# Performance work log

Measured on AMD Instinct MI355X. Metric: run time of the kernel, lower is better.

## Reference

```python
import jax, jax.numpy as jnp
import numpy as np

N_RAYS = 8192
N_SAMPLES = 64   # timesteps per ray
HID = 128
BOOSTER = 1.0
FAR = 10.0


def rsh_cart_3(d):
    # real spherical harmonics, cartesian, degree 3 -> 16 coefficients
    x, y, z = d[..., 0], d[..., 1], d[..., 2]
    x2, y2, z2 = x * x, y * y, z * z
    return jnp.stack([
        jnp.full_like(x, 0.282094791773878),
        -0.488602511902920 * y,
        0.488602511902920 * z,
        -0.488602511902920 * x,
        1.092548430592079 * x * y,
        -1.092548430592079 * y * z,
        0.315391565252520 * (3.0 * z2 - 1.0),
        -1.092548430592079 * x * z,
        0.546274215296040 * (x2 - y2),
        -0.590043589926644 * y * (3.0 * x2 - y2),
        2.890611442640554 * x * y * z,
        -0.457045799464466 * y * (5.0 * z2 - 1.0),
        0.373176332590115 * z * (5.0 * z2 - 3.0),
        -0.457045799464466 * x * (5.0 * z2 - 1.0),
        1.445305721320277 * z * (x2 - y2),
        -0.590043589926644 * x * (x2 - 3.0 * y2),
    ], axis=-1)


def setup_inputs() -> dict:
    key = jax.random.key(0)
    ks = jax.random.split(key, 10)
    N, H = N_RAYS, HID

    def w(k, shape, fan_in):
        return (jax.random.normal(k, shape, jnp.float32) / np.float32(np.sqrt(fan_in)))

    return dict(
        rays_o=jax.random.normal(ks[0], (N, 3), jnp.float32) * 0.3,
        rays_d=jax.random.normal(ks[1], (N, 3), jnp.float32),
        aabb=jnp.array([[-1.0, -1.0, -1.0], [1.0, 1.0, 1.0]], jnp.float32),
        W1=w(ks[2], (3, H), 3), b1=jnp.zeros((H,), jnp.float32),
        W2=w(ks[3], (H, H), H), b2=jnp.zeros((H,), jnp.float32),
        Wd=w(ks[4], (H, 1), H), bd=jnp.zeros((1,), jnp.float32),
        Wf=w(ks[5], (H, 16), H), bf=jnp.zeros((16,), jnp.float32),
        Wc1=w(ks[6], (32, H), 32), bc1=jnp.zeros((H,), jnp.float32),
        Wc2=w(ks[7], (H, 3), H), bc2=jnp.zeros((3,), jnp.float32),
    )


def reference(rays_o, rays_d, aabb, W1, b1, W2, b2, Wd, bd, Wf, bf, Wc1, bc1, Wc2, bc2):
    # --- ray / AABB intersection (slab test), as in RayBundle.intersect_aabb ---
    inv_d = 1.0 / rays_d
    t1 = (aabb[0] - rays_o) * inv_d
    t2 = (aabb[1] - rays_o) * inv_d
    tnear = jnp.maximum(jnp.max(jnp.minimum(t1, t2), -1), 0.0)      # (N,)
    tfar = jnp.minimum(jnp.min(jnp.maximum(t1, t2), -1), FAR)       # (N,)
    active = tnear < tfar                                           # active_mask()
    tnear = jnp.where(active, tnear, 0.0)
    tfar = jnp.where(active, tfar, 1.0)

    # --- timestep sampler: midpoint stratification between tnear/tfar ---
    T = N_SAMPLES
    frac = (jnp.arange(T, dtype=rays_o.dtype) + 0.5) / T
    ts = tnear[:, None] + frac[None, :] * (tfar - tnear)[:, None]    # (N,T)
    xyz = rays_o[:, None, :] + rays_d[:, None, :] * ts[..., None]    # (N,T,3)

    # --- convert_world_to_box_normalized + BoundsFilter.test ---
    xyz_ndc = (xyz - aabb[0]) / (aabb[1] - aabb[0]) * 2.0 - 1.0
    inside = jnp.all((xyz_ndc >= -1.0) & (xyz_ndc <= 1.0), -1)       # (N,T)

    # --- direction harmonics (rsh_cart_3 of normalized direction) ---
    dnorm = jnp.linalg.norm(rays_d, axis=-1, keepdims=True)          # (N,1)
    ynm = rsh_cart_3(rays_d / dnorm)                                 # (N,16)

    # --- radiance field MLP (query-everywhere; masked points contribute 0) ---
    h = jax.nn.relu(xyz_ndc @ W1 + b1)
    h = jax.nn.relu(h @ W2 + b2)
    sigma = jnp.exp(h @ Wd + bd)[..., 0]                             # (N,T) density
    feat = h @ Wf + bf                                               # (N,T,16)
    cond = jnp.broadcast_to(ynm[:, None, :], feat.shape)
    hc = jax.nn.relu(jnp.concatenate([feat, cond], -1) @ Wc1 + bc1)
    color = jax.nn.sigmoid(hc @ Wc2 + bc2)                           # (N,T,3)
    m = inside.astype(sigma.dtype)
    sigma = sigma * m                                                # scatter-zeros equiv
    color = color * m[..., None]

    # --- integrate_timesteps: transmittance * alpha weights ---
    tfinal = tfar + BOOSTER
    deltas = jnp.concatenate([ts[:, 1:] - ts[:, :-1], tfinal[:, None] - ts[:, -1:]], -1)
    tau = sigma * deltas * dnorm                                     # (N,T)
    excl = jnp.concatenate([jnp.zeros_like(tau[:, :1]), jnp.cumsum(tau[:, :-1], -1)], -1)
    weights = jnp.exp(-excl) * (1.0 - jnp.exp(-tau))                 # (N,T)

    # --- color_map / alpha_map / depth_map ---
    cmap = jnp.einsum('nt,ntc->nc', weights, color)                  # (N,3)
    amap = jnp.sum(weights, -1, keepdims=True)                       # (N,1)
    dmap = jnp.sum(weights * ts, -1, keepdims=True)                  # (N,1)
    am = active[:, None].astype(cmap.dtype)
    return jnp.concatenate([cmap * am, amap * am, dmap * am], -1)    # (N,5)
```

## Files before the change

### kernel.cpp

```cpp
#include <hip/hip_runtime.h>
#include <math.h>

#define THREADS 256
#define GRID 512
#define NRAYS 8192
#define FAR_T 10.0f
#define CSTR 24

typedef __attribute__((ext_vector_type(8))) short short8;
typedef __attribute__((ext_vector_type(4))) float f32x4;

static __device__ __forceinline__ unsigned f2bfu(float f) {
    unsigned u = __builtin_bit_cast(unsigned, f);
    return (u + 0x7fffu + ((u >> 16) & 1u)) >> 16;
}
static __device__ __forceinline__ unsigned pk2(float a, float b) {
    unsigned ra = __builtin_bit_cast(unsigned, a) + 0x8000u;
    unsigned rb = __builtin_bit_cast(unsigned, b) + 0x8000u;
    return __builtin_amdgcn_perm(rb, ra, 0x07060302u);
}
static __device__ __forceinline__ int sw128(int r, int k) { return (r << 7) + (k ^ ((r & 7) << 3)); }
static __device__ __forceinline__ int sw32(int r, int k)  { return (r << 5) + (k ^ ((r & 3) << 3)); }
static __device__ __forceinline__ f32x4 MFMA16(short8 a, short8 b, f32x4 c) {
    return __builtin_amdgcn_mfma_f32_16x16x32_bf16(a, b, c, 0, 0, 0);
}

struct RayP { float ox,oy,oz,dx,dy,dz,tn,tf,tstep,dnorm; bool act; };

static __device__ __forceinline__ RayP raySetup(const float* __restrict__ ro, const float* __restrict__ rd,
        int r, float a0x,float a0y,float a0z,float a1x,float a1y,float a1z) {
    RayP R;
    R.ox=ro[3*r+0]; R.oy=ro[3*r+1]; R.oz=ro[3*r+2];
    R.dx=rd[3*r+0]; R.dy=rd[3*r+1]; R.dz=rd[3*r+2];
    float ivx=1.f/R.dx, ivy=1.f/R.dy, ivz=1.f/R.dz;
    float t1x=(a0x-R.ox)*ivx, t2x=(a1x-R.ox)*ivx;
    float t1y=(a0y-R.oy)*ivy, t2y=(a1y-R.oy)*ivy;
    float t1z=(a0z-R.oz)*ivz, t2z=(a1z-R.oz)*ivz;
    float tn = fmaxf(fmaxf(fminf(t1x,t2x),fminf(t1y,t2y)),fminf(t1z,t2z));
    tn = fmaxf(tn, 0.f);
    float tf = fminf(fminf(fmaxf(t1x,t2x),fmaxf(t1y,t2y)),fmaxf(t1z,t2z));
    tf = fminf(tf, FAR_T);
    R.act = tn < tf;
    R.tn = R.act ? tn : 0.f;
    R.tf = R.act ? tf : 1.f;
    R.tstep = (R.tf - R.tn) * (1.f/64.f);
    R.dnorm = sqrtf(R.dx*R.dx + R.dy*R.dy + R.dz*R.dz);
    return R;
}

__global__ __launch_bounds__(THREADS)
__attribute__((amdgpu_waves_per_eu(2, 2), amdgpu_num_vgpr(256)))
void RadianceRenderer_kernel(const float* __restrict__ rays_o, const float* __restrict__ rays_d,
                             const float* __restrict__ aabb,
                             const float* __restrict__ W1, const float* __restrict__ b1,
                             const float* __restrict__ W2, const float* __restrict__ b2,
                             const float* __restrict__ Wd, const float* __restrict__ bd,
                             const float* __restrict__ Wf, const float* __restrict__ bf,
                             const float* __restrict__ Wc1, const float* __restrict__ bc1,
                             const float* __restrict__ Wc2, const float* __restrict__ bc2,
                             float* __restrict__ out)
{
    __shared__ __align__(16) short W1T[128*8];
    __shared__ __align__(16) short Wfd17[17*128];
    __shared__ __align__(16) short Wc2T3[3*128];
    __shared__ __align__(16) union {
        struct { short W2T[128*128]; short Wc1T[128*32]; } w;
        struct { short H1[128*128]; short H2[128*128]; short CC[128*CSTR];
                 short YNM[2*16]; float SIG[128]; float COL[128*4]; } a;
    } sm;

    const int tid  = threadIdx.x;
    const int lane = tid & 63;
    const int wv   = tid >> 6;
    const int l15  = lane & 15;
    const int l4   = lane >> 4;
    const short8 z8 = {0,0,0,0,0,0,0,0};

    for (int i = tid; i < 128*128; i += THREADS) {
        int k = i >> 7, n = i & 127;
        sm.w.W2T[sw128(n, k)] = (short)f2bfu(W2[i]);
    }
    for (int i = tid; i < 128*32; i += THREADS) {
        int n = i >> 5, k = i & 31;
        sm.w.Wc1T[sw32(n, k)] = (short)f2bfu(Wc1[k*128 + n]);
    }
    for (int i = tid; i < 17*128; i += THREADS) {
        int n = i >> 7, k = i & 127;
        float v = (n < 16) ? Wf[k*16 + n] : Wd[k];
        Wfd17[sw128(n, k)] = (short)f2bfu(v);
    }
    for (int i = tid; i < 3*128; i += THREADS) {
        int c = i >> 7, k = i & 127;
        Wc2T3[i] = (short)f2bfu(Wc2[k*3 + c]);
    }
    for (int i = tid; i < 128*8; i += THREADS) {
        int ch = i >> 3, k = i & 7;
        float f = (k < 3) ? W1[k*128 + ch] : ((k == 3) ? b1[ch] : 0.f);
        W1T[i] = (short)f2bfu(f);
    }
    __syncthreads();

    const int chB = (wv >> 1) * 64;
    const int smB = (wv & 1) * 64;
    const int sB3 = wv * 32;

    short8 w2f[4][4], wc1f[4];
    #pragma unroll
    for (int jn = 0; jn < 4; ++jn)
        #pragma unroll
        for (int kk = 0; kk < 4; ++kk)
            w2f[jn][kk] = *(const short8*)&sm.w.W2T[sw128(chB + 16*jn + l15, kk*32 + 8*l4)];
    #pragma unroll
    for (int cg = 0; cg < 4; ++cg)
        wc1f[cg] = *(const short8*)&sm.w.Wc1T[sw32(chB + 16*cg + l15, 8*l4)];

    float b2r[4][4], bc1r[4][4];
    #pragma unroll
    for (int jn = 0; jn < 4; ++jn)
        #pragma unroll
        for (int vv = 0; vv < 4; ++vv) {
            b2r[jn][vv]  = b2[chB + 16*jn + 4*l4 + vv];
            bc1r[jn][vv] = bc1[chB + 16*jn + 4*l4 + vv];
        }
    f32x4 bfv;
    #pragma unroll
    for (int vv = 0; vv < 4; ++vv) bfv[vv] = bf[4*l4 + vv];
    float bc2r[3] = { bc2[0], bc2[1], bc2[2] };
    const float bdr = bd[0];

    const float a0x=aabb[0],a0y=aabb[1],a0z=aabb[2],a1x=aabb[3],a1y=aabb[4],a1z=aabb[5];
    const float scx=2.f/(a1x-a0x), scy=2.f/(a1y-a0y), scz=2.f/(a1z-a0z);

    __syncthreads();

    for (int i = tid; i < 128*CSTR/2; i += THREADS) ((unsigned*)sm.a.CC)[i] = 0u;
    __syncthreads();

    int gp = -1;
    RayP Rp;

    for (int g = blockIdx.x; g < NRAYS/2; g += gridDim.x) {
        if (wv >= 2) {
            const int m   = tid - 128;
            const int ray = 2*g + (m >> 6);
            RayP R = raySetup(rays_o, rays_d, ray, a0x,a0y,a0z,a1x,a1y,a1z);
            const int s = m & 63;
            float t  = R.tn + ((float)s + 0.5f) * R.tstep;
            float px = fmaf(R.dx, t, R.ox);
            float py = fmaf(R.dy, t, R.oy);
            float pz = fmaf(R.dz, t, R.oz);
            float nx = fmaf(px - a0x, scx, -1.f);
            float ny = fmaf(py - a0y, scy, -1.f);
            float nz = fmaf(pz - a0z, scz, -1.f);
            *(uint2*)&sm.a.CC[m*CSTR] = make_uint2(pk2(nx, ny), pk2(nz, 1.0f));
            if (s == 0) {
                float inorm = 1.f / R.dnorm;
                float x = R.dx*inorm, y = R.dy*inorm, z = R.dz*inorm;
                float x2 = x*x, y2 = y*y, z2 = z*z;
                unsigned q0 = pk2(0.282094791773878f,              -0.488602511902920f*y);
                unsigned q1 = pk2(0.488602511902920f*z,            -0.488602511902920f*x);
                unsigned q2 = pk2(1.092548430592079f*x*y,          -1.092548430592079f*y*z);
                unsigned q3 = pk2(0.315391565252520f*(3.f*z2-1.f), -1.092548430592079f*x*z);
                unsigned q4 = pk2(0.546274215296040f*(x2-y2),      -0.590043589926644f*y*(3.f*x2-y2));
                unsigned q5 = pk2(2.890611442640554f*x*y*z,        -0.457045799464466f*y*(5.f*z2-1.f));
                unsigned q6 = pk2(0.373176332590115f*z*(5.f*z2-3.f), -0.457045799464466f*x*(5.f*z2-1.f));
                unsigned q7 = pk2(1.445305721320277f*z*(x2-y2),    -0.590043589926644f*x*(x2-3.f*y2));
                *(uint4*)&sm.a.YNM[(m >> 6)*16    ] = make_uint4(q0,q1,q2,q3);
                *(uint4*)&sm.a.YNM[(m >> 6)*16 + 8] = make_uint4(q4,q5,q6,q7);
            }
        } else if (gp >= 0) {
            const RayP R = Rp;
            const int m = wv*64 + lane;
            const int mx = (m >> 2) & 3;
            float t  = R.tn + ((float)lane + 0.5f) * R.tstep;
            float px = fmaf(R.dx, t, R.ox);
            float py = fmaf(R.dy, t, R.oy);
            float pz = fmaf(R.dz, t, R.oz);
            float nx = fmaf(px - a0x, scx, -1.f);
            float ny = fmaf(py - a0y, scy, -1.f);
            float nz = fmaf(pz - a0z, scz, -1.f);
            bool ins = (nx >= -1.f) & (nx <= 1.f) & (ny >= -1.f) & (ny <= 1.f)
                     & (nz >= -1.f) & (nz <= 1.f);
            float sig = ins ? __expf(sm.a.SIG[m] + bdr) : 0.f;
            float delta = (lane == 63) ? (R.tf + 1.0f - t) : R.tstep;
            float tau = sig * delta * R.dnorm;
            float cum = tau;
            #pragma unroll
            for (int off = 1; off < 64; off <<= 1) {
                float tmp = __shfl_up(cum, off);
                if (lane >= off) cum += tmp;
            }
            float excl = cum - tau;
            float wgt = __expf(-excl) * (1.f - __expf(-tau));
            float c0 = wgt * sm.a.COL[m*4 + (0 ^ mx)];
            float c1 = wgt * sm.a.COL[m*4 + (1 ^ mx)];
            float c2 = wgt * sm.a.COL[m*4 + (2 ^ mx)];
            float amv = wgt;
            float dmv = wgt * t;
            #pragma unroll
            for (int off = 32; off; off >>= 1) {
                c0  += __shfl_xor(c0,  off);
                c1  += __shfl_xor(c1,  off);
                c2  += __shfl_xor(c2,  off);
                amv += __shfl_xor(amv, off);
                dmv += __shfl_xor(dmv, off);
            }
            if (lane == 0) {
                float msk = R.act ? 1.f : 0.f;
                int ray = 2*gp + wv;
                out[ray*5+0] = c0*msk;
                out[ray*5+1] = c1*msk;
                out[ray*5+2] = c2*msk;
                out[ray*5+3] = amv*msk;
                out[ray*5+4] = dmv*msk;
            }
        }
        __syncthreads();

        {
            short8 bx[4];
            #pragma unroll
            for (int im = 0; im < 4; ++im) {
                short8 v = z8;
                if (l4 == 0) v = *(const short8*)&sm.a.CC[(smB + 16*im + l15)*CSTR];
                bx[im] = v;
            }
            #pragma unroll
            for (int jn = 0; jn < 4; ++jn) {
                short8 w1fr = z8;
                if (l4 == 0) w1fr = *(const short8*)&W1T[(chB + 16*jn + l15)*8];
                #pragma unroll
                for (int im = 0; im < 4; ++im) {
                    f32x4 v = MFMA16(w1fr, bx[im], (f32x4){0.f,0.f,0.f,0.f});
                    int m  = smB + 16*im + l15;
                    int n0 = chB + 16*jn + 4*l4;
                    float r0 = fmaxf(v[0], 0.f), r1 = fmaxf(v[1], 0.f);
                    float r2 = fmaxf(v[2], 0.f), r3 = fmaxf(v[3], 0.f);
                    *(uint2*)&sm.a.H1[sw128(m, n0)] = make_uint2(pk2(r0,r1), pk2(r2,r3));
                }
            }
        }
        __syncthreads();

        {
            f32x4 acc[4][4];
            #pragma unroll
            for (int jn = 0; jn < 4; ++jn)
                #pragma unroll
                for (int im = 0; im < 4; ++im)
                    acc[jn][im] = (f32x4){b2r[jn][0], b2r[jn][1], b2r[jn][2], b2r[jn][3]};
            #pragma unroll
            for (int kk = 0; kk < 4; ++kk) {
                short8 bfr[4];
                #pragma unroll
                for (int im = 0; im < 4; ++im)
                    bfr[im] = *(const short8*)&sm.a.H1[sw128(smB + 16*im + l15, kk*32 + 8*l4)];
                #pragma unroll
                for (int jn = 0; jn < 4; ++jn)
                    #pragma unroll
                    for (int im = 0; im < 4; ++im)
                        acc[jn][im] = MFMA16(w2f[jn][kk], bfr[im], acc[jn][im]);
            }
            #pragma unroll
            for (int jn = 0; jn < 4; ++jn)
                #pragma unroll
                for (int im = 0; im < 4; ++im) {
                    int m  = smB + 16*im + l15;
                    int n0 = chB + 16*jn + 4*l4;
                    f32x4 v = acc[jn][im];
                    float r0 = fmaxf(v[0], 0.f), r1 = fmaxf(v[1], 0.f);
                    float r2 = fmaxf(v[2], 0.f), r3 = fmaxf(v[3], 0.f);
                    *(uint2*)&sm.a.H2[sw128(m, n0)] = make_uint2(pk2(r0,r1), pk2(r2,r3));
                }
        }
        __syncthreads();

        {
            f32x4 f30[2] = { bfv, bfv };
            f32x4 f31[2] = { (f32x4){0,0,0,0}, (f32x4){0,0,0,0} };
            #pragma unroll
            for (int kk = 0; kk < 4; ++kk) {
                short8 bA = *(const short8*)&sm.a.H2[sw128(sB3 +      l15, kk*32 + 8*l4)];
                short8 bB = *(const short8*)&sm.a.H2[sw128(sB3 + 16 + l15, kk*32 + 8*l4)];
                short8 wfd0 = *(const short8*)&Wfd17[sw128(l15, kk*32 + 8*l4)];
                short8 wfd1 = z8;
                if (l15 == 0) wfd1 = *(const short8*)&Wfd17[sw128(16, kk*32 + 8*l4)];
                f30[0] = MFMA16(wfd0, bA, f30[0]);
                f30[1] = MFMA16(wfd0, bB, f30[1]);
                f31[0] = MFMA16(wfd1, bA, f31[0]);
                f31[1] = MFMA16(wfd1, bB, f31[1]);
            }
            #pragma unroll
            for (int sg = 0; sg < 2; ++sg) {
                int m = sB3 + 16*sg + l15;
                f32x4 v = f30[sg];
                *(uint2*)&sm.a.CC[m*CSTR + 4*l4] = make_uint2(pk2(v[0],v[1]), pk2(v[2],v[3]));
                if (l4 == 0) sm.a.SIG[m] = f31[sg][0];
            }
        }
        __syncthreads();

        {
            short8 bcc[4];
            #pragma unroll
            for (int sg = 0; sg < 4; ++sg) {
                int m = smB + 16*sg + l15;
                if (l4 < 2) bcc[sg] = *(const short8*)&sm.a.CC[m*CSTR + 8*l4];
                else        bcc[sg] = *(const short8*)&sm.a.YNM[(m >> 6)*16 + 8*(l4 - 2)];
            }
            #pragma unroll
            for (int cg = 0; cg < 4; ++cg)
                #pragma unroll
                for (int sg = 0; sg < 4; ++sg) {
                    f32x4 v = MFMA16(wc1f[cg], bcc[sg],
                                     (f32x4){bc1r[cg][0], bc1r[cg][1], bc1r[cg][2], bc1r[cg][3]});
                    int m  = smB + 16*sg + l15;
                    int n0 = chB + 16*cg + 4*l4;
                    float r0 = fmaxf(v[0], 0.f), r1 = fmaxf(v[1], 0.f);
                    float r2 = fmaxf(v[2], 0.f), r3 = fmaxf(v[3], 0.f);
                    *(uint2*)&sm.a.H1[sw128(m, n0)] = make_uint2(pk2(r0,r1), pk2(r2,r3));
                }
        }
        __syncthreads();

        {
            f32x4 c5[2] = { (f32x4){0,0,0,0}, (f32x4){0,0,0,0} };
            #pragma unroll
            for (int kk = 0; kk < 4; ++kk) {
                short8 wc2fr = z8;
                if (l15 < 3) wc2fr = *(const short8*)&Wc2T3[l15*128 + kk*32 + 8*l4];
                #pragma unroll
                for (int sg = 0; sg < 2; ++sg) {
                    short8 b = *(const short8*)&sm.a.H1[sw128(sB3 + 16*sg + l15, kk*32 + 8*l4)];
                    c5[sg] = MFMA16(wc2fr, b, c5[sg]);
                }
            }
            if (l4 == 0) {
                #pragma unroll
                for (int sg = 0; sg < 2; ++sg) {
                    int m = sB3 + 16*sg + l15;
                    int mx = (m >> 2) & 3;
                    #pragma unroll
                    for (int vv = 0; vv < 3; ++vv)
                        sm.a.COL[m*4 + (vv ^ mx)] = 1.f / (1.f + __expf(-(c5[sg][vv] + bc2r[vv])));
                }
            }
        }
        __syncthreads();

        if (wv < 2) Rp = raySetup(rays_o, rays_d, 2*g + wv, a0x,a0y,a0z,a1x,a1y,a1z);
        gp = g;
    }

    if (gp >= 0 && wv < 2) {
        const RayP R = Rp;
        const int m = wv*64 + lane;
        const int mx = (m >> 2) & 3;
        float t  = R.tn + ((float)lane + 0.5f) * R.tstep;
        float px = fmaf(R.dx, t, R.ox);
        float py = fmaf(R.dy, t, R.oy);
        float pz = fmaf(R.dz, t, R.oz);
        float nx = fmaf(px - a0x, scx, -1.f);
        float ny = fmaf(py - a0y, scy, -1.f);
        float nz = fmaf(pz - a0z, scz, -1.f);
        bool ins = (nx >= -1.f) & (nx <= 1.f) & (ny >= -1.f) & (ny <= 1.f)
                 & (nz >= -1.f) & (nz <= 1.f);
        float sig = ins ? __expf(sm.a.SIG[m] + bdr) : 0.f;
        float delta = (lane == 63) ? (R.tf + 1.0f - t) : R.tstep;
        float tau = sig * delta * R.dnorm;
        float cum = tau;
        #pragma unroll
        for (int off = 1; off < 64; off <<= 1) {
            float tmp = __shfl_up(cum, off);
            if (lane >= off) cum += tmp;
        }
        float excl = cum - tau;
        float wgt = __expf(-excl) * (1.f - __expf(-tau));
        float c0 = wgt * sm.a.COL[m*4 + (0 ^ mx)];
        float c1 = wgt * sm.a.COL[m*4 + (1 ^ mx)];
        float c2 = wgt * sm.a.COL[m*4 + (2 ^ mx)];
        float amv = wgt;
        float dmv = wgt * t;
        #pragma unroll
        for (int off = 32; off; off >>= 1) {
            c0  += __shfl_xor(c0,  off);
            c1  += __shfl_xor(c1,  off);
            c2  += __shfl_xor(c2,  off);
            amv += __shfl_xor(amv, off);
            dmv += __shfl_xor(dmv, off);
        }
        if (lane == 0) {
            float msk = R.act ? 1.f : 0.f;
            int ray = 2*gp + wv;
            out[ray*5+0] = c0*msk;
            out[ray*5+1] = c1*msk;
            out[ray*5+2] = c2*msk;
            out[ray*5+3] = amv*msk;
            out[ray*5+4] = dmv*msk;
        }
    }
}

extern "C" void kernel_launch(void* const* d_in, const int* in_sizes, int n_in,
                              void* d_out, int out_size, void* d_ws, size_t ws_size,
                              hipStream_t stream) {
    (void)in_sizes; (void)n_in; (void)d_ws; (void)ws_size; (void)out_size;
    const float* rays_o = (const float*)d_in[0];
    const float* rays_d = (const float*)d_in[1];
    const float* aabb   = (const float*)d_in[2];
    const float* W1  = (const float*)d_in[3];
    const float* b1  = (const float*)d_in[4];
    const float* W2  = (const float*)d_in[5];
    const float* b2  = (const float*)d_in[6];
    const float* Wd  = (const float*)d_in[7];
    const float* bd  = (const float*)d_in[8];
    const float* Wf  = (const float*)d_in[9];
    const float* bf  = (const float*)d_in[10];
    const float* Wc1 = (const float*)d_in[11];
    const float* bc1 = (const float*)d_in[12];
    const float* Wc2 = (const float*)d_in[13];
    const float* bc2 = (const float*)d_in[14];
    float* out = (float*)d_out;

    hipLaunchKernelGGL(RadianceRenderer_kernel, dim3(GRID), dim3(THREADS), 0, stream,
                       rays_o, rays_d, aabb, W1, b1, W2, b2, Wd, bd,
                       Wf, bf, Wc1, bc1, Wc2, bc2, out);
}
```

Before: 164.9 us.

## Double block to 512 threads, halve per-wave MFMA tiles, move biases to LDS

Raises the block from 4 to 8 waves and splits each GEMM's output channels across twice as many waves, so each wave holds half as many W2/Wc1 fragments and accumulators. Bias vectors now live in shared memory instead of registers. Color and sigma are stored in a planar CS array, and the SH coefficients are folded into unused CC padding. The ray setup is recomputed instead of carried across iterations. The goal is lower register pressure and more waves to hide latency, at the cost of more LDS traffic and idle waves in the per-ray stages.

```diff
diff --git a/kernel.cpp b/kernel.cpp
--- a/kernel.cpp
+++ b/kernel.cpp
@@ -1,7 +1,7 @@
 #include <hip/hip_runtime.h>
 #include <math.h>
 
-#define THREADS 256
+#define THREADS 512
 #define GRID 512
 #define NRAYS 8192
 #define FAR_T 10.0f
@@ -48,8 +48,7 @@
     return R;
 }
 
-__global__ __launch_bounds__(THREADS)
-__attribute__((amdgpu_waves_per_eu(2, 2), amdgpu_num_vgpr(256)))
+__global__ __launch_bounds__(THREADS, 4)
 void RadianceRenderer_kernel(const float* __restrict__ rays_o, const float* __restrict__ rays_d,
                              const float* __restrict__ aabb,
                              const float* __restrict__ W1, const float* __restrict__ b1,
@@ -63,10 +62,13 @@
     __shared__ __align__(16) short W1T[128*8];
     __shared__ __align__(16) short Wfd17[17*128];
     __shared__ __align__(16) short Wc2T3[3*128];
+    __shared__ __align__(16) float B2F[128];
+    __shared__ __align__(16) float BC1F[128];
     __shared__ __align__(16) union {
         struct { short W2T[128*128]; short Wc1T[128*32]; } w;
-        struct { short H1[128*128]; short H2[128*128]; short CC[128*CSTR];
-                 short YNM[2*16]; float SIG[128]; float COL[128*4]; } a;
+        struct { short H1[128*128]; short H2[128*128];
+                 short CC[128*CSTR];
+                 float CS[4*128]; } a;
     } sm;
 
     const int tid  = threadIdx.x;
@@ -98,30 +100,23 @@
         float f = (k < 3) ? W1[k*128 + ch] : ((k == 3) ? b1[ch] : 0.f);
         W1T[i] = (short)f2bfu(f);
     }
+    for (int i = tid; i < 128; i += THREADS) { B2F[i] = b2[i]; BC1F[i] = bc1[i]; }
     __syncthreads();
 
-    const int chB = (wv >> 1) * 64;
+    const int chB = (wv >> 1) * 32;
     const int smB = (wv & 1) * 64;
-    const int sB3 = wv * 32;
-
-    short8 w2f[4][4], wc1f[4];
+    const int sB3 = wv * 16;
+
+    short8 w2f[2][4], wc1f[2];
     #pragma unroll
-    for (int jn = 0; jn < 4; ++jn)
+    for (int jn = 0; jn < 2; ++jn)
         #pragma unroll
         for (int kk = 0; kk < 4; ++kk)
             w2f[jn][kk] = *(const short8*)&sm.w.W2T[sw128(chB + 16*jn + l15, kk*32 + 8*l4)];
     #pragma unroll
-    for (int cg = 0; cg < 4; ++cg)
+    for (int cg = 0; cg < 2; ++cg)
         wc1f[cg] = *(const short8*)&sm.w.Wc1T[sw32(chB + 16*cg + l15, 8*l4)];
 
-    float b2r[4][4], bc1r[4][4];
-    #pragma unroll
-    for (int jn = 0; jn < 4; ++jn)
-        #pragma unroll
-        for (int vv = 0; vv < 4; ++vv) {
-            b2r[jn][vv]  = b2[chB + 16*jn + 4*l4 + vv];
-            bc1r[jn][vv] = bc1[chB + 16*jn + 4*l4 + vv];
-        }
     f32x4 bfv;
     #pragma unroll
     for (int vv = 0; vv < 4; ++vv) bfv[vv] = bf[4*l4 + vv];
@@ -137,11 +132,10 @@
     __syncthreads();
 
     int gp = -1;
-    RayP Rp;
 
     for (int g = blockIdx.x; g < NRAYS/2; g += gridDim.x) {
-        if (wv >= 2) {
-            const int m   = tid - 128;
+        if (wv == 4 || wv == 5) {
+            const int m   = tid - 256;
             const int ray = 2*g + (m >> 6);
             RayP R = raySetup(rays_o, rays_d, ray, a0x,a0y,a0z,a1x,a1y,a1z);
             const int s = m & 63;
@@ -165,13 +159,12 @@
                 unsigned q5 = pk2(2.890611442640554f*x*y*z,        -0.457045799464466f*y*(5.f*z2-1.f));
                 unsigned q6 = pk2(0.373176332590115f*z*(5.f*z2-3.f), -0.457045799464466f*x*(5.f*z2-1.f));
                 unsigned q7 = pk2(1.445305721320277f*z*(x2-y2),    -0.590043589926644f*x*(x2-3.f*y2));
-                *(uint4*)&sm.a.YNM[(m >> 6)*16    ] = make_uint4(q0,q1,q2,q3);
-                *(uint4*)&sm.a.YNM[(m >> 6)*16 + 8] = make_uint4(q4,q5,q6,q7);
-            }
-        } else if (gp >= 0) {
-            const RayP R = Rp;
+                *(uint4*)&sm.a.CC[m*CSTR + 16]        = make_uint4(q0,q1,q2,q3);
+                *(uint4*)&sm.a.CC[(m+1)*CSTR + 16]    = make_uint4(q4,q5,q6,q7);
+            }
+        } else if (wv < 2 && gp >= 0) {
+            RayP R = raySetup(rays_o, rays_d, 2*gp + wv, a0x,a0y,a0z,a1x,a1y,a1z);
             const int m = wv*64 + lane;
-            const int mx = (m >> 2) & 3;
             float t  = R.tn + ((float)lane + 0.5f) * R.tstep;
             float px = fmaf(R.dx, t, R.ox);
             float py = fmaf(R.dy, t, R.oy);
@@ -181,7 +174,7 @@
             float nz = fmaf(pz - a0z, scz, -1.f);
             bool ins = (nx >= -1.f) & (nx <= 1.f) & (ny >= -1.f) & (ny <= 1.f)
                      & (nz >= -1.f) & (nz <= 1.f);
-            float sig = ins ? __expf(sm.a.SIG[m] + bdr) : 0.f;
+            float sig = ins ? __expf(sm.a.CS[3*128 + m] + bdr) : 0.f;
             float delta = (lane == 63) ? (R.tf + 1.0f - t) : R.tstep;
             float tau = sig * delta * R.dnorm;
             float cum = tau;
@@ -192,9 +185,9 @@
             }
             float excl = cum - tau;
             float wgt = __expf(-excl) * (1.f - __expf(-tau));
-            float c0 = wgt * sm.a.COL[m*4 + (0 ^ mx)];
-            float c1 = wgt * sm.a.COL[m*4 + (1 ^ mx)];
-            float c2 = wgt * sm.a.COL[m*4 + (2 ^ mx)];
+            float c0 = wgt * sm.a.CS[0*128 + m];
+            float c1 = wgt * sm.a.CS[1*128 + m];
+            float c2 = wgt * sm.a.CS[2*128 + m];
             float amv = wgt;
             float dmv = wgt * t;
             #pragma unroll
@@ -226,7 +219,7 @@
                 bx[im] = v;
             }
             #pragma unroll
-            for (int jn = 0; jn < 4; ++jn) {
+            for (int jn = 0; jn < 2; ++jn) {
                 short8 w1fr = z8;
                 if (l4 == 0) w1fr = *(const short8*)&W1T[(chB + 16*jn + l15)*8];
                 #pragma unroll
@@ -243,26 +236,23 @@
         __syncthreads();
 
         {
-            f32x4 acc[4][4];
-            #pragma unroll
-            for (int jn = 0; jn < 4; ++jn)
-                #pragma unroll
-                for (int im = 0; im < 4; ++im)
-                    acc[jn][im] = (f32x4){b2r[jn][0], b2r[jn][1], b2r[jn][2], b2r[jn][3]};
-            #pragma unroll
-            for (int kk = 0; kk < 4; ++kk) {
-                short8 bfr[4];
-                #pragma unroll
-                for (int im = 0; im < 4; ++im)
-                    bfr[im] = *(const short8*)&sm.a.H1[sw128(smB + 16*im + l15, kk*32 + 8*l4)];
-                #pragma unroll
-                for (int jn = 0; jn < 4; ++jn)
-                    #pragma unroll
-                    for (int im = 0; im < 4; ++im)
-                        acc[jn][im] = MFMA16(w2f[jn][kk], bfr[im], acc[jn][im]);
-            }
-            #pragma unroll
-            for (int jn = 0; jn < 4; ++jn)
+            f32x4 acc[2][4];
+            #pragma unroll
+            for (int jn = 0; jn < 2; ++jn) {
+                f32x4 bias = *(const f32x4*)&B2F[chB + 16*jn + 4*l4];
+                #pragma unroll
+                for (int im = 0; im < 4; ++im) acc[jn][im] = bias;
+            }
+            #pragma unroll
+            for (int kk = 0; kk < 4; ++kk)
+                #pragma unroll
+                for (int im = 0; im < 4; ++im) {
+                    short8 bfr = *(const short8*)&sm.a.H1[sw128(smB + 16*im + l15, kk*32 + 8*l4)];
+                    acc[0][im] = MFMA16(w2f[0][kk], bfr, acc[0][im]);
+                    acc[1][im] = MFMA16(w2f[1][kk], bfr, acc[1][im]);
+                }
+            #pragma unroll
+            for (int jn = 0; jn < 2; ++jn)
                 #pragma unroll
                 for (int im = 0; im < 4; ++im) {
                     int m  = smB + 16*im + l15;
@@ -276,27 +266,20 @@
         __syncthreads();
 
         {
-            f32x4 f30[2] = { bfv, bfv };
-            f32x4 f31[2] = { (f32x4){0,0,0,0}, (f32x4){0,0,0,0} };
+            f32x4 f30 = bfv;
+            f32x4 f31 = (f32x4){0.f,0.f,0.f,0.f};
+            const int m = sB3 + l15;
             #pragma unroll
             for (int kk = 0; kk < 4; ++kk) {
-                short8 bA = *(const short8*)&sm.a.H2[sw128(sB3 +      l15, kk*32 + 8*l4)];
-                short8 bB = *(const short8*)&sm.a.H2[sw128(sB3 + 16 + l15, kk*32 + 8*l4)];
+                short8 bA = *(const short8*)&sm.a.H2[sw128(m, kk*32 + 8*l4)];
                 short8 wfd0 = *(const short8*)&Wfd17[sw128(l15, kk*32 + 8*l4)];
                 short8 wfd1 = z8;
                 if (l15 == 0) wfd1 = *(const short8*)&Wfd17[sw128(16, kk*32 + 8*l4)];
-                f30[0] = MFMA16(wfd0, bA, f30[0]);
-                f30[1] = MFMA16(wfd0, bB, f30[1]);
-                f31[0] = MFMA16(wfd1, bA, f31[0]);
-                f31[1] = MFMA16(wfd1, bB, f31[1]);
-            }
-            #pragma unroll
-            for (int sg = 0; sg < 2; ++sg) {
-                int m = sB3 + 16*sg + l15;
-                f32x4 v = f30[sg];
-                *(uint2*)&sm.a.CC[m*CSTR + 4*l4] = make_uint2(pk2(v[0],v[1]), pk2(v[2],v[3]));
-                if (l4 == 0) sm.a.SIG[m] = f31[sg][0];
-            }
+                f30 = MFMA16(wfd0, bA, f30);
+                f31 = MFMA16(wfd1, bA, f31);
+            }
+            *(uint2*)&sm.a.CC[m*CSTR + 4*l4] = make_uint2(pk2(f30[0],f30[1]), pk2(f30[2],f30[3]));
+            if (l4 == 0) sm.a.CS[3*128 + m] = f31[0];
         }
         __syncthreads();
 
@@ -306,56 +289,48 @@
             for (int sg = 0; sg < 4; ++sg) {
                 int m = smB + 16*sg + l15;
                 if (l4 < 2) bcc[sg] = *(const short8*)&sm.a.CC[m*CSTR + 8*l4];
-                else        bcc[sg] = *(const short8*)&sm.a.YNM[(m >> 6)*16 + 8*(l4 - 2)];
-            }
-            #pragma unroll
-            for (int cg = 0; cg < 4; ++cg)
+                else        bcc[sg] = *(const short8*)&sm.a.CC[((m >> 6)*64 + (l4 - 2))*CSTR + 16];
+            }
+            #pragma unroll
+            for (int cg = 0; cg < 2; ++cg) {
+                f32x4 bias = *(const f32x4*)&BC1F[chB + 16*cg + 4*l4];
                 #pragma unroll
                 for (int sg = 0; sg < 4; ++sg) {
-                    f32x4 v = MFMA16(wc1f[cg], bcc[sg],
-                                     (f32x4){bc1r[cg][0], bc1r[cg][1], bc1r[cg][2], bc1r[cg][3]});
+                    f32x4 v = MFMA16(wc1f[cg], bcc[sg], bias);
                     int m  = smB + 16*sg + l15;
                     int n0 = chB + 16*cg + 4*l4;
                     float r0 = fmaxf(v[0], 0.f), r1 = fmaxf(v[1], 0.f);
                     float r2 = fmaxf(v[2], 0.f), r3 = fmaxf(v[3], 0.f);
                     *(uint2*)&sm.a.H1[sw128(m, n0)] = make_uint2(pk2(r0,r1), pk2(r2,r3));
                 }
+            }
         }
         __syncthreads();
 
         {
-            f32x4 c5[2] = { (f32x4){0,0,0,0}, (f32x4){0,0,0,0} };
+            f32x4 c5 = (f32x4){0.f,0.f,0.f,0.f};
+            const int m = sB3 + l15;
             #pragma unroll
             for (int kk = 0; kk < 4; ++kk) {
                 short8 wc2fr = z8;
                 if (l15 < 3) wc2fr = *(const short8*)&Wc2T3[l15*128 + kk*32 + 8*l4];
-                #pragma unroll
-                for (int sg = 0; sg < 2; ++sg) {
-                    short8 b = *(const short8*)&sm.a.H1[sw128(sB3 + 16*sg + l15, kk*32 + 8*l4)];
-                    c5[sg] = MFMA16(wc2fr, b, c5[sg]);
-                }
+                short8 b = *(const short8*)&sm.a.H1[sw128(m, kk*32 + 8*l4)];
+                c5 = MFMA16(wc2fr, b, c5);
             }
             if (l4 == 0) {
                 #pragma unroll
-                for (int sg = 0; sg < 2; ++sg) {
-                    int m = sB3 + 16*sg + l15;
-                    int mx = (m >> 2) & 3;
-                    #pragma unroll
-                    for (int vv = 0; vv < 3; ++vv)
-                        sm.a.COL[m*4 + (vv ^ mx)] = 1.f / (1.f + __expf(-(c5[sg][vv] + bc2r[vv])));
-                }
-            }
-        }
-        __syncthreads();
-
-        if (wv < 2) Rp = raySetup(rays_o, rays_d, 2*g + wv, a0x,a0y,a0z,a1x,a1y,a1z);
+                for (int vv = 0; vv < 3; ++vv)
+                    sm.a.CS[vv*128 + m] = 1.f / (1.f + __expf(-(c5[vv] + bc2r[vv])));
+            }
+        }
+        __syncthreads();
+
         gp = g;
     }
 
     if (gp >= 0 && wv < 2) {
-        const RayP R = Rp;
+        RayP R = raySetup(rays_o, rays_d, 2*gp + wv, a0x,a0y,a0z,a1x,a1y,a1z);
         const int m = wv*64 + lane;
-        const int mx = (m >> 2) & 3;
         float t  = R.tn + ((float)lane + 0.5f) * R.tstep;
         float px = fmaf(R.dx, t, R.ox);
         float py = fmaf(R.dy, t, R.oy);
@@ -365,7 +340,7 @@
         float nz = fmaf(pz - a0z, scz, -1.f);
         bool ins = (nx >= -1.f) & (nx <= 1.f) & (ny >= -1.f) & (ny <= 1.f)
                  & (nz >= -1.f) & (nz <= 1.f);
-        float sig = ins ? __expf(sm.a.SIG[m] + bdr) : 0.f;
+        float sig = ins ? __expf(sm.a.CS[3*128 + m] + bdr) : 0.f;
         float delta = (lane == 63) ? (R.tf + 1.0f - t) : R.tstep;
         float tau = sig * delta * R.dnorm;
         float cum = tau;
@@ -376,9 +351,9 @@
         }
         float excl = cum - tau;
         float wgt = __expf(-excl) * (1.f - __expf(-tau));
-        float c0 = wgt * sm.a.COL[m*4 + (0 ^ mx)];
-        float c1 = wgt * sm.a.COL[m*4 + (1 ^ mx)];
-        float c2 = wgt * sm.a.COL[m*4 + (2 ^ mx)];
+        float c0 = wgt * sm.a.CS[0*128 + m];
+        float c1 = wgt * sm.a.CS[1*128 + m];
+        float c2 = wgt * sm.a.CS[2*128 + m];
         float amv = wgt;
         float dmv = wgt * t;
         #pragma unroll
```

Measured after the change: 147.9 us. 10.3% less time.
